# Optimization experiments

Measured on AMD Instinct MI355X. Metric: run time of the kernel, lower is better.

## Reference

```python
import jax, jax.numpy as jnp
import numpy as np

ENC, TAG, LANG, ATT = 512, 512, 512, 256
N, P = 1024, 1024


def setup_inputs() -> dict:
    key = jax.random.key(0)
    ks = jax.random.split(key, 11)
    s = lambda d: 1.0 / np.sqrt(d)
    return {
        "encoder_out": jax.random.normal(ks[0], (1, P, ENC), jnp.float32),
        "decoder_hidden": jax.random.normal(ks[1], (N, TAG), jnp.float32),
        "language_out": jax.random.normal(ks[2], (N, LANG), jnp.float32),
        "We": jax.random.uniform(ks[3], (ATT, ENC), jnp.float32, -s(ENC), s(ENC)),
        "be": jax.random.uniform(ks[4], (ATT,), jnp.float32, -s(ENC), s(ENC)),
        "Wt": jax.random.uniform(ks[5], (ATT, TAG), jnp.float32, -s(TAG), s(TAG)),
        "bt": jax.random.uniform(ks[6], (ATT,), jnp.float32, -s(TAG), s(TAG)),
        "Wl": jax.random.uniform(ks[7], (ATT, LANG), jnp.float32, -s(LANG), s(LANG)),
        "bl": jax.random.uniform(ks[8], (ATT,), jnp.float32, -s(LANG), s(LANG)),
        "Wf": jax.random.uniform(ks[9], (1, ATT), jnp.float32, -s(ATT), s(ATT)),
        "bf": jax.random.uniform(ks[10], (1,), jnp.float32, -s(ATT), s(ATT)),
    }


def reference(encoder_out, decoder_hidden, language_out, We, be, Wt, bt, Wl, bl, Wf, bf):
    # att1: (1, P, A); att2, att3: (N, A)
    att1 = jnp.einsum("bpe,ae->bpa", encoder_out, We) + be
    att2 = decoder_hidden @ Wt.T + bt
    att3 = language_out @ Wl.T + bl
    # broadcast add -> (N, P, A), relu, reduce to scalar score per pixel
    h = jax.nn.relu(att1 + (att2 + att3)[:, None, :])  # (N, P, A)
    att = jnp.einsum("npa,a->np", h, Wf[0]) + bf[0]     # (N, P)
    alpha = jax.nn.softmax(att, axis=1)
    # softmax-weighted sum over pixels -> (N, ENC)
    awe = jnp.einsum("np,pe->ne", alpha, encoder_out[0])
    return awe, alpha
```

## Files before the change

### kernel.cpp

```cpp
#include <hip/hip_runtime.h>
#include <hip/hip_bf16.h>
#include <math.h>

#define ENC 512
#define ATT 256
#define NN 1024
#define PP 1024

typedef __attribute__((ext_vector_type(8))) __bf16 bf16x8;
typedef __attribute__((ext_vector_type(4))) float floatx4;
typedef __attribute__((ext_vector_type(2))) float floatx2;

union LdsVec { uint4 u; bf16x8 v; };

__device__ __forceinline__ unsigned cvt_pk(float lo, float hi) {
    union { __hip_bfloat162 h; unsigned u; } x;
    x.h = __float22bfloat162_rn(float2{lo, hi});
    return x.u;
}
__device__ __forceinline__ uint4 cvt8(float4 f0, float4 f1) {
    uint4 r;
    r.x = cvt_pk(f0.x, f0.y); r.y = cvt_pk(f0.z, f0.w);
    r.z = cvt_pk(f1.x, f1.y); r.w = cvt_pk(f1.z, f1.w);
    return r;
}
__device__ __forceinline__ float2 bfpair(unsigned w) {
    union { unsigned u; float f; } lo, hi;
    lo.u = w << 16; hi.u = w & 0xffff0000u;
    return float2{lo.f, hi.f};
}

__device__ __forceinline__ int tile_off(int row, int k) {
    return row * 32 + ((((k >> 3) ^ ((row >> 1) & 3)) & 3) << 3) + (k & 7);
}

__global__ __launch_bounds__(256) void mfma_uv(
    const float* __restrict__ E,  const float* __restrict__ We, const float* __restrict__ be,
    const float* __restrict__ D,  const float* __restrict__ Wt, const float* __restrict__ bt,
    const float* __restrict__ Lg, const float* __restrict__ Wl, const float* __restrict__ bl,
    unsigned short* __restrict__ uT, unsigned short* __restrict__ v1T,
    unsigned short* __restrict__ v2T, unsigned short* __restrict__ ET)
{
    const int tid = threadIdx.x;

    if (blockIdx.z == 3) {
        __shared__ unsigned short T[64][72];
        const int k0 = blockIdx.y * 64;
        const int kr = tid >> 2, nc = (tid & 3) * 16;
        const int nr = tid >> 2, kc = (tid & 3) * 16;
        #pragma unroll
        for (int t = 0; t < 2; ++t) {
            const int n0 = (blockIdx.x * 2 + t) * 64;
            const float* ep = E + (size_t)(k0 + kr) * ENC + n0 + nc;
            float4 a = *(const float4*)(ep + 0),  b = *(const float4*)(ep + 4);
            float4 c = *(const float4*)(ep + 8),  d = *(const float4*)(ep + 12);
            if (t) __syncthreads();
            *(uint4*)&T[kr][nc]     = cvt8(a, b);
            *(uint4*)&T[kr][nc + 8] = cvt8(c, d);
            __syncthreads();
            unsigned short tmp[16];
            #pragma unroll
            for (int i = 0; i < 16; ++i) tmp[i] = T[kc + i][nr];
            unsigned short* op = ET + (size_t)(n0 + nr) * PP + k0 + kc;
            *(uint4*)(op)     = *(uint4*)&tmp[0];
            *(uint4*)(op + 8) = *(uint4*)&tmp[8];
        }
        return;
    }

    __shared__ __align__(16) unsigned short As[2][64 * 32];
    __shared__ __align__(16) unsigned short Bs[2][64 * 32];
    const int K = 512;

    const float *A, *B, *bias; unsigned short* out;
    if      (blockIdx.z == 0) { A = E;  B = We; bias = be; out = uT;  }
    else if (blockIdx.z == 1) { A = D;  B = Wt; bias = bt; out = v1T; }
    else                      { A = Lg; B = Wl; bias = bl; out = v2T; }

    const int m0 = blockIdx.y * 64, n0 = blockIdx.x * 64;
    const int wv = tid >> 6, lm = tid & 15, lq = (tid >> 4) & 3;
    const int mb = (wv & 1) * 32, nb = (wv >> 1) * 32;
    const int a0o = tile_off(mb + lm,      lq * 8);
    const int a1o = tile_off(mb + 16 + lm, lq * 8);
    const int b0o = tile_off(nb + lm,      lq * 8);
    const int b1o = tile_off(nb + 16 + lm, lq * 8);

    const int row = tid >> 2, kseg = tid & 3;
    const int soff = tile_off(row, kseg * 8);
    const float* Ap = A + (size_t)(m0 + row) * K + kseg * 8;
    const float* Bp = B + (size_t)(n0 + row) * K + kseg * 8;

    floatx4 acc[2][2];
    const floatx4 zero = {0.f, 0.f, 0.f, 0.f};
    acc[0][0] = zero; acc[0][1] = zero; acc[1][0] = zero; acc[1][1] = zero;

    float4 pa0 = *(const float4*)(Ap), pa1 = *(const float4*)(Ap + 4);
    float4 pb0 = *(const float4*)(Bp), pb1 = *(const float4*)(Bp + 4);

    for (int k0 = 0; k0 < K; k0 += 32) {
        const int buf = (k0 >> 5) & 1;
        *(uint4*)&As[buf][soff] = cvt8(pa0, pa1);
        *(uint4*)&Bs[buf][soff] = cvt8(pb0, pb1);
        __syncthreads();
        if (k0 + 32 < K) {
            pa0 = *(const float4*)(Ap + k0 + 32); pa1 = *(const float4*)(Ap + k0 + 36);
            pb0 = *(const float4*)(Bp + k0 + 32); pb1 = *(const float4*)(Bp + k0 + 36);
        }
        LdsVec fa0, fa1, fb0, fb1;
        fa0.u = *(const uint4*)&As[buf][a0o];
        fa1.u = *(const uint4*)&As[buf][a1o];
        fb0.u = *(const uint4*)&Bs[buf][b0o];
        fb1.u = *(const uint4*)&Bs[buf][b1o];
        acc[0][0] = __builtin_amdgcn_mfma_f32_16x16x32_bf16(fa0.v, fb0.v, acc[0][0], 0, 0, 0);
        acc[0][1] = __builtin_amdgcn_mfma_f32_16x16x32_bf16(fa0.v, fb1.v, acc[0][1], 0, 0, 0);
        acc[1][0] = __builtin_amdgcn_mfma_f32_16x16x32_bf16(fa1.v, fb0.v, acc[1][0], 0, 0, 0);
        acc[1][1] = __builtin_amdgcn_mfma_f32_16x16x32_bf16(fa1.v, fb1.v, acc[1][1], 0, 0, 0);
    }

    #pragma unroll
    for (int s = 0; s < 2; ++s) {
        const int col = n0 + nb + s * 16 + lm;
        const float bsum = bias[col];
        #pragma unroll
        for (int t = 0; t < 2; ++t) {
            const int mbase = m0 + mb + t * 16 + lq * 4;
            uint2 o;
            o.x = cvt_pk(acc[t][s][0] + bsum, acc[t][s][1] + bsum);
            o.y = cvt_pk(acc[t][s][2] + bsum, acc[t][s][3] + bsum);
            *(uint2*)&out[(size_t)col * NN + mbase] = o;
        }
    }
}

__global__ __launch_bounds__(256) void att_fused(
    const unsigned short* __restrict__ uT, const unsigned short* __restrict__ v1T,
    const unsigned short* __restrict__ v2T,
    const float* __restrict__ Wf, float* __restrict__ att_part)
{
    __shared__ float us[32][132];
    __shared__ float vs[32][68];
    __shared__ float wfs[128];
    const int tid = threadIdx.x;
    const int z = blockIdx.z;
    if (tid < 128) wfs[tid] = Wf[z * 128 + tid];
    const int p0 = blockIdx.x * 128, n0 = blockIdx.y * 64;
    const int arow = tid >> 3, t8 = tid & 7;
    const int pcol = t8 * 16, ncol = t8 * 8;
    const int tx = tid & 15, ty = tid >> 4;

    floatx2 acc[4][4];
    const floatx2 z2 = {0.f, 0.f};
    #pragma unroll
    for (int j = 0; j < 4; ++j)
        #pragma unroll
        for (int h = 0; h < 4; ++h) acc[j][h] = z2;

    const int abase = z * 128;
    for (int ac = 0; ac < 128; ac += 32) {
        __syncthreads();
        {
            const size_t arow_g = (size_t)(abase + ac + arow) * NN;
            const unsigned short* up = uT + arow_g + p0 + pcol;
            uint4 ua = *(const uint4*)up;
            uint4 ub = *(const uint4*)(up + 8);
            float* ud = &us[arow][pcol];
            float2 c;
            c = bfpair(ua.x); ud[0] = c.x; ud[1] = c.y;
            c = bfpair(ua.y); ud[2] = c.x; ud[3] = c.y;
            c = bfpair(ua.z); ud[4] = c.x; ud[5] = c.y;
            c = bfpair(ua.w); ud[6] = c.x; ud[7] = c.y;
            c = bfpair(ub.x); ud[8] = c.x; ud[9] = c.y;
            c = bfpair(ub.y); ud[10] = c.x; ud[11] = c.y;
            c = bfpair(ub.z); ud[12] = c.x; ud[13] = c.y;
            c = bfpair(ub.w); ud[14] = c.x; ud[15] = c.y;
            uint4 va = *(const uint4*)(v1T + arow_g + n0 + ncol);
            uint4 vb = *(const uint4*)(v2T + arow_g + n0 + ncol);
            float* vd = &vs[arow][ncol];
            float2 a0, b0;
            a0 = bfpair(va.x); b0 = bfpair(vb.x); vd[0] = a0.x + b0.x; vd[1] = a0.y + b0.y;
            a0 = bfpair(va.y); b0 = bfpair(vb.y); vd[2] = a0.x + b0.x; vd[3] = a0.y + b0.y;
            a0 = bfpair(va.z); b0 = bfpair(vb.z); vd[4] = a0.x + b0.x; vd[5] = a0.y + b0.y;
            a0 = bfpair(va.w); b0 = bfpair(vb.w); vd[6] = a0.x + b0.x; vd[7] = a0.y + b0.y;
        }
        __syncthreads();
        #pragma unroll
        for (int a = 0; a < 32; ++a) {
            float4 u0 = *(const float4*)&us[a][tx * 4];
            float4 u1 = *(const float4*)&us[a][tx * 4 + 64];
            float4 v4 = *(const float4*)&vs[a][ty * 4];
            const float w = wfs[ac + a];
            floatx2 u00 = {u0.x, u0.y}, u01 = {u0.z, u0.w};
            floatx2 u10 = {u1.x, u1.y}, u11 = {u1.z, u1.w};
            const float vv[4] = {v4.x, v4.y, v4.z, v4.w};
            #pragma unroll
            for (int j = 0; j < 4; ++j) {
                floatx2 t0 = __builtin_elementwise_max(u00 + vv[j], z2);
                floatx2 t1 = __builtin_elementwise_max(u01 + vv[j], z2);
                floatx2 t2 = __builtin_elementwise_max(u10 + vv[j], z2);
                floatx2 t3 = __builtin_elementwise_max(u11 + vv[j], z2);
                acc[j][0] = t0 * w + acc[j][0];
                acc[j][1] = t1 * w + acc[j][1];
                acc[j][2] = t2 * w + acc[j][2];
                acc[j][3] = t3 * w + acc[j][3];
            }
        }
    }

    float* outp = att_part + (size_t)z * NN * PP;
    #pragma unroll
    for (int j = 0; j < 4; ++j) {
        float* rowp = &outp[(size_t)(n0 + ty * 4 + j) * PP + p0];
        float4 o;
        o.x = acc[j][0].x; o.y = acc[j][0].y; o.z = acc[j][1].x; o.w = acc[j][1].y;
        *(float4*)&rowp[tx * 4] = o;
        o.x = acc[j][2].x; o.y = acc[j][2].y; o.z = acc[j][3].x; o.w = acc[j][3].y;
        *(float4*)&rowp[tx * 4 + 64] = o;
    }
}

__global__ __launch_bounds__(256) void softmax_rows(
    const float* __restrict__ att_part, float* __restrict__ alpha,
    unsigned short* __restrict__ alpha_bf)
{
    const int wv = threadIdx.x >> 6, lane = threadIdx.x & 63;
    const int n = blockIdx.x * 4 + wv;
    const float* r0 = att_part + (size_t)n * PP;
    const float* r1 = att_part + (size_t)NN * PP + (size_t)n * PP;

    float4 x[4];
    #pragma unroll
    for (int i = 0; i < 4; ++i) {
        float4 a = *(const float4*)&r0[i * 256 + lane * 4];
        float4 b = *(const float4*)&r1[i * 256 + lane * 4];
        x[i].x = a.x + b.x; x[i].y = a.y + b.y; x[i].z = a.z + b.z; x[i].w = a.w + b.w;
    }

    float m = -1e30f;
    #pragma unroll
    for (int i = 0; i < 4; ++i)
        m = fmaxf(m, fmaxf(fmaxf(x[i].x, x[i].y), fmaxf(x[i].z, x[i].w)));
    #pragma unroll
    for (int off = 32; off > 0; off >>= 1) m = fmaxf(m, __shfl_xor(m, off, 64));

    float s = 0.f;
    #pragma unroll
    for (int i = 0; i < 4; ++i) {
        x[i].x = __expf(x[i].x - m); x[i].y = __expf(x[i].y - m);
        x[i].z = __expf(x[i].z - m); x[i].w = __expf(x[i].w - m);
        s += x[i].x + x[i].y + x[i].z + x[i].w;
    }
    #pragma unroll
    for (int off = 32; off > 0; off >>= 1) s += __shfl_xor(s, off, 64);
    const float inv = 1.0f / s;

    float* ar = alpha + (size_t)n * PP;
    unsigned short* br = alpha_bf + (size_t)n * PP;
    #pragma unroll
    for (int i = 0; i < 4; ++i) {
        x[i].x *= inv; x[i].y *= inv; x[i].z *= inv; x[i].w *= inv;
        *(float4*)&ar[i * 256 + lane * 4] = x[i];
        uint2 pk;
        pk.x = cvt_pk(x[i].x, x[i].y);
        pk.y = cvt_pk(x[i].z, x[i].w);
        *(uint2*)&br[i * 256 + lane * 4] = pk;
    }
}

__global__ __launch_bounds__(256) void mfma_awe(
    const unsigned short* __restrict__ alpha_bf,
    const unsigned short* __restrict__ ET, float* __restrict__ awe)
{
    __shared__ __align__(16) unsigned short As[2][32 * 32];
    __shared__ __align__(16) unsigned short Bs[2][64 * 32];
    const int tid = threadIdx.x;
    const int K = PP;
    const int m0 = blockIdx.y * 32, n0 = blockIdx.x * 64;
    const int wv = tid >> 6, lm = tid & 15, lq = (tid >> 4) & 3;
    const int mw = (wv & 1) * 16, nw = (wv >> 1) * 32;
    const int a0o = tile_off(mw + lm,      lq * 8);
    const int b0o = tile_off(nw + lm,      lq * 8);
    const int b1o = tile_off(nw + 16 + lm, lq * 8);

    const int rowA = tid >> 3, kcA = (tid & 7) * 4;
    const int rowB = tid >> 2, kcB = (tid & 3) * 8;
    const int aoff = tile_off(rowA, kcA);
    const int boff = tile_off(rowB, kcB);
    const unsigned short* Ap = alpha_bf + (size_t)(m0 + rowA) * PP + kcA;
    const unsigned short* Bp = ET + (size_t)(n0 + rowB) * PP + kcB;

    floatx4 acc[2];
    const floatx4 zero = {0.f, 0.f, 0.f, 0.f};
    acc[0] = zero; acc[1] = zero;

    uint2 pa = *(const uint2*)Ap;
    uint4 pb = *(const uint4*)Bp;

    for (int k0 = 0; k0 < K; k0 += 32) {
        const int buf = (k0 >> 5) & 1;
        *(uint2*)&As[buf][aoff] = pa;
        *(uint4*)&Bs[buf][boff] = pb;
        __syncthreads();
        if (k0 + 32 < K) {
            pa = *(const uint2*)(Ap + k0 + 32);
            pb = *(const uint4*)(Bp + k0 + 32);
        }
        LdsVec fa, fb0, fb1;
        fa.u  = *(const uint4*)&As[buf][a0o];
        fb0.u = *(const uint4*)&Bs[buf][b0o];
        fb1.u = *(const uint4*)&Bs[buf][b1o];
        acc[0] = __builtin_amdgcn_mfma_f32_16x16x32_bf16(fa.v, fb0.v, acc[0], 0, 0, 0);
        acc[1] = __builtin_amdgcn_mfma_f32_16x16x32_bf16(fa.v, fb1.v, acc[1], 0, 0, 0);
    }

    #pragma unroll
    for (int s = 0; s < 2; ++s) {
        const int col = n0 + nw + s * 16 + lm;
        #pragma unroll
        for (int r = 0; r < 4; ++r)
            awe[(size_t)(m0 + mw + lq * 4 + r) * ENC + col] = acc[s][r];
    }
}

extern "C" void kernel_launch(void* const* d_in, const int* in_sizes, int n_in,
                              void* d_out, int out_size, void* d_ws, size_t ws_size,
                              hipStream_t stream)
{
    const float* encoder = (const float*)d_in[0];
    const float* dec     = (const float*)d_in[1];
    const float* lang    = (const float*)d_in[2];
    const float* We      = (const float*)d_in[3];
    const float* be      = (const float*)d_in[4];
    const float* Wt      = (const float*)d_in[5];
    const float* bt      = (const float*)d_in[6];
    const float* Wl      = (const float*)d_in[7];
    const float* bl      = (const float*)d_in[8];
    const float* Wf      = (const float*)d_in[9];

    unsigned short* uT  = (unsigned short*)d_ws;
    unsigned short* v1T = uT  + ATT * NN;
    unsigned short* v2T = v1T + ATT * NN;
    float* attp = (float*)(v2T + ATT * NN);
    unsigned short* alpha_bf = (unsigned short*)(attp + 2 * (size_t)NN * PP);
    unsigned short* ET       = alpha_bf + (size_t)NN * PP;

    float* awe   = (float*)d_out;
    float* alpha = (float*)d_out + NN * ENC;

    mfma_uv<<<dim3(4, 16, 4), 256, 0, stream>>>(
        encoder, We, be, dec, Wt, bt, lang, Wl, bl, uT, v1T, v2T, ET);
    att_fused<<<dim3(PP / 128, NN / 64, 2), 256, 0, stream>>>(uT, v1T, v2T, Wf, attp);
    softmax_rows<<<dim3(NN / 4), 256, 0, stream>>>(attp, alpha, alpha_bf);
    mfma_awe<<<dim3(ENC / 64, NN / 32), 256, 0, stream>>>(alpha_bf, ET, awe);
}
```

Measured before the change: 127.2 us.

## Fuse softmax into the score kernel with deferred normalization in the awe GEMM

The score kernel now covers the whole attention dimension in one pass, removing the split partials. It exponentiates scores directly without subtracting the row max, stores the exponentials as bf16 and accumulates row sums with atomics into a workspace buffer that the first kernel zeroes. The separate softmax kernel is removed. The awe GEMM divides its output by the row sums and also writes normalized alpha from the bf16 exponentials. This avoids writing and re-reading fp32 partial scores and one kernel launch. In exchange it risks exp overflow for large scores and lowers alpha precision, since alpha is rebuilt from bf16 values.

```diff
diff --git a/kernel.cpp b/kernel.cpp
--- a/kernel.cpp
+++ b/kernel.cpp
@@ -39,11 +39,16 @@
     const float* __restrict__ D,  const float* __restrict__ Wt, const float* __restrict__ bt,
     const float* __restrict__ Lg, const float* __restrict__ Wl, const float* __restrict__ bl,
     unsigned short* __restrict__ uT, unsigned short* __restrict__ v1T,
-    unsigned short* __restrict__ v2T, unsigned short* __restrict__ ET)
+    unsigned short* __restrict__ v2T, unsigned short* __restrict__ ET,
+    float* __restrict__ S)
 {
     const int tid = threadIdx.x;
 
     if (blockIdx.z == 3) {
+        if (blockIdx.x == 0 && blockIdx.y == 0) {
+            const floatx4 z4 = {0.f, 0.f, 0.f, 0.f};
+            *(floatx4*)&S[tid * 4] = z4;
+        }
         __shared__ unsigned short T[64][72];
         const int k0 = blockIdx.y * 64;
         const int kr = tid >> 2, nc = (tid & 3) * 16;
@@ -132,50 +137,40 @@
     }
 }
 
-__global__ __launch_bounds__(256) void att_fused(
+__global__ __launch_bounds__(256) void att_exp(
     const unsigned short* __restrict__ uT, const unsigned short* __restrict__ v1T,
     const unsigned short* __restrict__ v2T,
-    const float* __restrict__ Wf, float* __restrict__ att_part)
+    const float* __restrict__ Wf,
+    unsigned short* __restrict__ expv, float* __restrict__ S)
 {
-    __shared__ float us[32][132];
+    __shared__ float us[32][68];
     __shared__ float vs[32][68];
-    __shared__ float wfs[128];
+    __shared__ float wfs[ATT];
     const int tid = threadIdx.x;
-    const int z = blockIdx.z;
-    if (tid < 128) wfs[tid] = Wf[z * 128 + tid];
-    const int p0 = blockIdx.x * 128, n0 = blockIdx.y * 64;
-    const int arow = tid >> 3, t8 = tid & 7;
-    const int pcol = t8 * 16, ncol = t8 * 8;
+    wfs[tid] = Wf[tid];
+    const int p0 = blockIdx.x * 64, n0 = blockIdx.y * 64;
+    const int rowS = tid >> 3, cS = (tid & 7) * 8;
     const int tx = tid & 15, ty = tid >> 4;
 
-    floatx2 acc[4][4];
+    floatx2 acc[4][2];
     const floatx2 z2 = {0.f, 0.f};
     #pragma unroll
-    for (int j = 0; j < 4; ++j)
-        #pragma unroll
-        for (int h = 0; h < 4; ++h) acc[j][h] = z2;
-
-    const int abase = z * 128;
-    for (int ac = 0; ac < 128; ac += 32) {
+    for (int j = 0; j < 4; ++j) { acc[j][0] = z2; acc[j][1] = z2; }
+
+    for (int ac = 0; ac < ATT; ac += 32) {
         __syncthreads();
         {
-            const size_t arow_g = (size_t)(abase + ac + arow) * NN;
-            const unsigned short* up = uT + arow_g + p0 + pcol;
-            uint4 ua = *(const uint4*)up;
-            uint4 ub = *(const uint4*)(up + 8);
-            float* ud = &us[arow][pcol];
+            const size_t arow_g = (size_t)(ac + rowS) * NN;
+            uint4 ua = *(const uint4*)(uT + arow_g + p0 + cS);
+            float* ud = &us[rowS][cS];
             float2 c;
             c = bfpair(ua.x); ud[0] = c.x; ud[1] = c.y;
             c = bfpair(ua.y); ud[2] = c.x; ud[3] = c.y;
             c = bfpair(ua.z); ud[4] = c.x; ud[5] = c.y;
             c = bfpair(ua.w); ud[6] = c.x; ud[7] = c.y;
-            c = bfpair(ub.x); ud[8] = c.x; ud[9] = c.y;
-            c = bfpair(ub.y); ud[10] = c.x; ud[11] = c.y;
-            c = bfpair(ub.z); ud[12] = c.x; ud[13] = c.y;
-            c = bfpair(ub.w); ud[14] = c.x; ud[15] = c.y;
-            uint4 va = *(const uint4*)(v1T + arow_g + n0 + ncol);
-            uint4 vb = *(const uint4*)(v2T + arow_g + n0 + ncol);
-            float* vd = &vs[arow][ncol];
+            uint4 va = *(const uint4*)(v1T + arow_g + n0 + cS);
+            uint4 vb = *(const uint4*)(v2T + arow_g + n0 + cS);
+            float* vd = &vs[rowS][cS];
             float2 a0, b0;
             a0 = bfpair(va.x); b0 = bfpair(vb.x); vd[0] = a0.x + b0.x; vd[1] = a0.y + b0.y;
             a0 = bfpair(va.y); b0 = bfpair(vb.y); vd[2] = a0.x + b0.x; vd[3] = a0.y + b0.y;
@@ -185,90 +180,44 @@
         __syncthreads();
         #pragma unroll
         for (int a = 0; a < 32; ++a) {
-            float4 u0 = *(const float4*)&us[a][tx * 4];
-            float4 u1 = *(const float4*)&us[a][tx * 4 + 64];
+            float4 u4 = *(const float4*)&us[a][tx * 4];
             float4 v4 = *(const float4*)&vs[a][ty * 4];
             const float w = wfs[ac + a];
-            floatx2 u00 = {u0.x, u0.y}, u01 = {u0.z, u0.w};
-            floatx2 u10 = {u1.x, u1.y}, u11 = {u1.z, u1.w};
+            floatx2 ulo = {u4.x, u4.y}, uhi = {u4.z, u4.w};
             const float vv[4] = {v4.x, v4.y, v4.z, v4.w};
             #pragma unroll
             for (int j = 0; j < 4; ++j) {
-                floatx2 t0 = __builtin_elementwise_max(u00 + vv[j], z2);
-                floatx2 t1 = __builtin_elementwise_max(u01 + vv[j], z2);
-                floatx2 t2 = __builtin_elementwise_max(u10 + vv[j], z2);
-                floatx2 t3 = __builtin_elementwise_max(u11 + vv[j], z2);
+                floatx2 t0 = __builtin_elementwise_max(ulo + vv[j], z2);
+                floatx2 t1 = __builtin_elementwise_max(uhi + vv[j], z2);
                 acc[j][0] = t0 * w + acc[j][0];
                 acc[j][1] = t1 * w + acc[j][1];
-                acc[j][2] = t2 * w + acc[j][2];
-                acc[j][3] = t3 * w + acc[j][3];
             }
         }
     }
 
-    float* outp = att_part + (size_t)z * NN * PP;
     #pragma unroll
     for (int j = 0; j < 4; ++j) {
-        float* rowp = &outp[(size_t)(n0 + ty * 4 + j) * PP + p0];
-        float4 o;
-        o.x = acc[j][0].x; o.y = acc[j][0].y; o.z = acc[j][1].x; o.w = acc[j][1].y;
-        *(float4*)&rowp[tx * 4] = o;
-        o.x = acc[j][2].x; o.y = acc[j][2].y; o.z = acc[j][3].x; o.w = acc[j][3].y;
-        *(float4*)&rowp[tx * 4 + 64] = o;
-    }
-}
-
-__global__ __launch_bounds__(256) void softmax_rows(
-    const float* __restrict__ att_part, float* __restrict__ alpha,
-    unsigned short* __restrict__ alpha_bf)
-{
-    const int wv = threadIdx.x >> 6, lane = threadIdx.x & 63;
-    const int n = blockIdx.x * 4 + wv;
-    const float* r0 = att_part + (size_t)n * PP;
-    const float* r1 = att_part + (size_t)NN * PP + (size_t)n * PP;
-
-    float4 x[4];
-    #pragma unroll
-    for (int i = 0; i < 4; ++i) {
-        float4 a = *(const float4*)&r0[i * 256 + lane * 4];
-        float4 b = *(const float4*)&r1[i * 256 + lane * 4];
-        x[i].x = a.x + b.x; x[i].y = a.y + b.y; x[i].z = a.z + b.z; x[i].w = a.w + b.w;
-    }
-
-    float m = -1e30f;
-    #pragma unroll
-    for (int i = 0; i < 4; ++i)
-        m = fmaxf(m, fmaxf(fmaxf(x[i].x, x[i].y), fmaxf(x[i].z, x[i].w)));
-    #pragma unroll
-    for (int off = 32; off > 0; off >>= 1) m = fmaxf(m, __shfl_xor(m, off, 64));
-
-    float s = 0.f;
-    #pragma unroll
-    for (int i = 0; i < 4; ++i) {
-        x[i].x = __expf(x[i].x - m); x[i].y = __expf(x[i].y - m);
-        x[i].z = __expf(x[i].z - m); x[i].w = __expf(x[i].w - m);
-        s += x[i].x + x[i].y + x[i].z + x[i].w;
-    }
-    #pragma unroll
-    for (int off = 32; off > 0; off >>= 1) s += __shfl_xor(s, off, 64);
-    const float inv = 1.0f / s;
-
-    float* ar = alpha + (size_t)n * PP;
-    unsigned short* br = alpha_bf + (size_t)n * PP;
-    #pragma unroll
-    for (int i = 0; i < 4; ++i) {
-        x[i].x *= inv; x[i].y *= inv; x[i].z *= inv; x[i].w *= inv;
-        *(float4*)&ar[i * 256 + lane * 4] = x[i];
+        const int n = n0 + ty * 4 + j;
+        float e0 = __expf(acc[j][0].x), e1 = __expf(acc[j][0].y);
+        float e2 = __expf(acc[j][1].x), e3 = __expf(acc[j][1].y);
+        float s = (e0 + e1) + (e2 + e3);
+        s += __shfl_xor(s, 1, 64);
+        s += __shfl_xor(s, 2, 64);
+        s += __shfl_xor(s, 4, 64);
+        s += __shfl_xor(s, 8, 64);
+        if (tx == 0) atomicAdd(&S[n], s);
         uint2 pk;
-        pk.x = cvt_pk(x[i].x, x[i].y);
-        pk.y = cvt_pk(x[i].z, x[i].w);
-        *(uint2*)&br[i * 256 + lane * 4] = pk;
+        pk.x = cvt_pk(e0, e1);
+        pk.y = cvt_pk(e2, e3);
+        *(uint2*)&expv[(size_t)n * PP + p0 + tx * 4] = pk;
     }
 }
 
 __global__ __launch_bounds__(256) void mfma_awe(
-    const unsigned short* __restrict__ alpha_bf,
-    const unsigned short* __restrict__ ET, float* __restrict__ awe)
+    const unsigned short* __restrict__ expv,
+    const unsigned short* __restrict__ ET,
+    const float* __restrict__ S,
+    float* __restrict__ awe, float* __restrict__ alpha)
 {
     __shared__ __align__(16) unsigned short As[2][32 * 32];
     __shared__ __align__(16) unsigned short Bs[2][64 * 32];
@@ -285,7 +234,7 @@
     const int rowB = tid >> 2, kcB = (tid & 3) * 8;
     const int aoff = tile_off(rowA, kcA);
     const int boff = tile_off(rowB, kcB);
-    const unsigned short* Ap = alpha_bf + (size_t)(m0 + rowA) * PP + kcA;
+    const unsigned short* Ap = expv + (size_t)(m0 + rowA) * PP + kcA;
     const unsigned short* Bp = ET + (size_t)(n0 + rowB) * PP + kcB;
 
     floatx4 acc[2];
@@ -312,12 +261,38 @@
         acc[1] = __builtin_amdgcn_mfma_f32_16x16x32_bf16(fa.v, fb1.v, acc[1], 0, 0, 0);
     }
 
+    float inv[4];
+    #pragma unroll
+    for (int r = 0; r < 4; ++r) inv[r] = 1.0f / S[m0 + mw + lq * 4 + r];
+
     #pragma unroll
     for (int s = 0; s < 2; ++s) {
         const int col = n0 + nw + s * 16 + lm;
         #pragma unroll
         for (int r = 0; r < 4; ++r)
-            awe[(size_t)(m0 + mw + lq * 4 + r) * ENC + col] = acc[s][r];
+            awe[(size_t)(m0 + mw + lq * 4 + r) * ENC + col] = acc[s][r] * inv[r];
+    }
+
+    if (blockIdx.x == 0) {
+        const int r = tid >> 3;
+        const int c0 = (tid & 7) * 128;
+        const int rown = m0 + r;
+        const float rinv = 1.0f / S[rown];
+        const unsigned short* ep = expv + (size_t)rown * PP + c0;
+        float* ap = alpha + (size_t)rown * PP + c0;
+        #pragma unroll
+        for (int i = 0; i < 128; i += 8) {
+            uint4 w = *(const uint4*)&ep[i];
+            float2 c0v = bfpair(w.x), c1v = bfpair(w.y);
+            float2 c2v = bfpair(w.z), c3v = bfpair(w.w);
+            float4 o0, o1;
+            o0.x = c0v.x * rinv; o0.y = c0v.y * rinv;
+            o0.z = c1v.x * rinv; o0.w = c1v.y * rinv;
+            o1.x = c2v.x * rinv; o1.y = c2v.y * rinv;
+            o1.z = c3v.x * rinv; o1.w = c3v.y * rinv;
+            *(float4*)&ap[i]     = o0;
+            *(float4*)&ap[i + 4] = o1;
+        }
     }
 }
 
@@ -336,19 +311,18 @@
     const float* bl      = (const float*)d_in[8];
     const float* Wf      = (const float*)d_in[9];
 
-    unsigned short* uT  = (unsigned short*)d_ws;
-    unsigned short* v1T = uT  + ATT * NN;
-    unsigned short* v2T = v1T + ATT * NN;
-    float* attp = (float*)(v2T + ATT * NN);
-    unsigned short* alpha_bf = (unsigned short*)(attp + 2 * (size_t)NN * PP);
-    unsigned short* ET       = alpha_bf + (size_t)NN * PP;
+    unsigned short* uT   = (unsigned short*)d_ws;
+    unsigned short* v1T  = uT  + ATT * NN;
+    unsigned short* v2T  = v1T + ATT * NN;
+    unsigned short* ET   = v2T + ATT * NN;
+    unsigned short* expv = ET + (size_t)ENC * PP;
+    float* S             = (float*)(expv + (size_t)NN * PP);
 
     float* awe   = (float*)d_out;
     float* alpha = (float*)d_out + NN * ENC;
 
     mfma_uv<<<dim3(4, 16, 4), 256, 0, stream>>>(
-        encoder, We, be, dec, Wt, bt, lang, Wl, bl, uT, v1T, v2T, ET);
-    att_fused<<<dim3(PP / 128, NN / 64, 2), 256, 0, stream>>>(uT, v1T, v2T, Wf, attp);
-    softmax_rows<<<dim3(NN / 4), 256, 0, stream>>>(attp, alpha, alpha_bf);
-    mfma_awe<<<dim3(ENC / 64, NN / 32), 256, 0, stream>>>(alpha_bf, ET, awe);
-}
+        encoder, We, be, dec, Wt, bt, lang, Wl, bl, uT, v1T, v2T, ET, S);
+    att_exp<<<dim3(PP / 64, NN / 64), 256, 0, stream>>>(uT, v1T, v2T, Wf, expv, S);
+    mfma_awe<<<dim3(ENC / 64, NN / 32), 256, 0, stream>>>(expv, ET, S, awe, alpha);
+}
```

After: 143.3 us. 1.13x slower.
